# Kernel optimization log

Hardware: AMD Instinct MI355X
Metric: run time of the kernel (lower is better)

The kernel has to match this reference:

```python
import jax, jax.numpy as jnp
import numpy as np

B, N, M, K = 4, 2048, 8192, 3          # batches, coarse pts/batch, fine pts/batch, knn k
C_IN, C_SKIP, H, C_OUT = 256, 128, 256, 128


def setup_inputs() -> dict:
    key = jax.random.key(0)
    ks = jax.random.split(key, 8)
    x = jax.random.normal(ks[0], (B * N, C_IN), jnp.float32)
    pos = jax.random.normal(ks[1], (B * N, 3), jnp.float32)
    batch = jnp.repeat(jnp.arange(B, dtype=jnp.int64), N)        # sorted, equal-sized batches
    x_skip = jax.random.normal(ks[2], (B * M, C_SKIP), jnp.float32)
    pos_skip = jax.random.normal(ks[3], (B * M, 3), jnp.float32)
    batch_skip = jnp.repeat(jnp.arange(B, dtype=jnp.int64), M)
    # MLP params: Linear(384->256) + ReLU + Linear(256->128)
    W1 = jax.random.normal(ks[4], (C_IN + C_SKIP, H), jnp.float32) / np.sqrt(C_IN + C_SKIP)
    b1 = jnp.zeros((H,), jnp.float32)
    W2 = jax.random.normal(ks[5], (H, C_OUT), jnp.float32) / np.sqrt(H)
    b2 = jnp.zeros((C_OUT,), jnp.float32)
    return {"x": x, "pos": pos, "x_skip": x_skip, "pos_skip": pos_skip,
            "W1": W1, "b1": b1, "W2": W2, "b2": b2,
            "batch": batch, "batch_skip": batch_skip}


def _knn_interpolate(x, pos, pos_skip):
    # x: [B*N, C], pos: [B*N, 3], pos_skip: [B*M, 3]; batches are equal-sized & sorted,
    # so per-batch kNN == reshape to [B, n, ...] (matches batch/batch_skip vectors).
    xb = x.reshape(B, N, C_IN)
    pb = pos.reshape(B, N, 3)
    qb = pos_skip.reshape(B, M, 3)
    # squared pairwise distances via GEMM expansion: [B, M, N]
    d2 = (jnp.sum(qb * qb, -1)[:, :, None]
          + jnp.sum(pb * pb, -1)[:, None, :]
          - 2.0 * jnp.einsum('bmd,bnd->bmn', qb, pb))
    neg_d2, idx = jax.lax.top_k(-d2, K)           # k smallest distances
    d2k = jnp.maximum(-neg_d2, 0.0)               # [B, M, K]
    w = 1.0 / (d2k + 1e-16)                       # inverse-squared-distance weights
    feats = xb[jnp.arange(B)[:, None, None], idx] # gather: [B, M, K, C]
    interp = jnp.sum(w[..., None] * feats, axis=2) / jnp.sum(w, axis=2)[..., None]
    return interp.reshape(B * M, C_IN)


def reference(x, pos, x_skip, pos_skip, W1, b1, W2, b2, batch, batch_skip):
    xi = _knn_interpolate(x, pos, pos_skip)              # [B*M, C_IN]
    h = jnp.concatenate([xi, x_skip], axis=1)            # [B*M, C_IN+C_SKIP]
    h = jax.nn.relu(h @ W1 + b1)
    out = h @ W2 + b2                                    # [B*M, C_OUT]
    return (out, pos_skip, batch_skip)
```

## Files before the change

kernel.cpp:

```cpp
#include <hip/hip_runtime.h>
#include <math.h>
#include <stdint.h>

#define Bn    4
#define Nn    2048
#define Mn    8192
#define CIN   256
#define CSKIP 128
#define HID   256
#define COUT  128
#define KTOT  384

typedef short bf16x8 __attribute__((ext_vector_type(8)));
typedef float f32x16 __attribute__((ext_vector_type(16)));

__device__ __forceinline__ ushort f2bf(float f) {
    union { float f; unsigned u; } v; v.f = f;
    return (ushort)((v.u + 0x7fffu + ((v.u >> 16) & 1u)) >> 16);
}

__global__ __launch_bounds__(256) void pack_pos4(
    const float* __restrict__ pos, float4* __restrict__ pos4)
{
    const int i = blockIdx.x * 256 + threadIdx.x;
    const float* p = pos + (size_t)i * 3;
    const float p0 = p[0], p1 = p[1], p2 = p[2];
    const float pp = __fadd_rn(__fadd_rn(__fmul_rn(p0, p0), __fmul_rn(p1, p1)),
                               __fmul_rn(p2, p2));
    pos4[i] = make_float4(2.0f * p0, 2.0f * p1, 2.0f * p2, pp);
}

#define INSERT3(kA, kB, kC, k)            \
    do {                                  \
        const double _t = fmax(kA, k);    \
        kA = fmin(kA, k);                 \
        const double _u = fmax(kB, _t);   \
        kB = fmin(kB, _t);                \
        kC = fmin(kC, _u);                \
    } while (0)

__global__ __launch_bounds__(256) void fused_mid(
    const float* __restrict__ x,
    const float4* __restrict__ pos4,
    const float* __restrict__ xs,
    const float* __restrict__ pos_skip,
    const float* __restrict__ W1, const float* __restrict__ W2,
    ushort* __restrict__ Abig,
    ushort* __restrict__ W1T, ushort* __restrict__ W2T,
    float* __restrict__ tail_dst)
{
    __shared__ double sKey[16][3][17];
    __shared__ int    sIdx[16][3];
    __shared__ float  sRW[16][3];

    const int bid = blockIdx.x;
    const int tid = threadIdx.x;

    if (bid >= 2048) {
        const int cb = bid - 2048;
        if (cb < 4096) {
            const int q   = cb * 256 + tid;
            const int row = q >> 5;
            const int cq  = (q & 31) * 4;
            const float4 v = *(const float4*)(xs + (size_t)row * CSKIP + cq);
            ushort4 o; o.x = f2bf(v.x); o.y = f2bf(v.y); o.z = f2bf(v.z); o.w = f2bf(v.w);
            *(ushort4*)(Abig + (size_t)row * KTOT + CIN + cq) = o;
        } else if (cb < 4192) {
            const int q  = (cb - 4096) * 256 + tid;
            const int n  = q / 96;
            const int kq = (q % 96) * 4;
            ushort4 o;
            o.x = f2bf(W1[(size_t)(kq + 0) * HID + n]);
            o.y = f2bf(W1[(size_t)(kq + 1) * HID + n]);
            o.z = f2bf(W1[(size_t)(kq + 2) * HID + n]);
            o.w = f2bf(W1[(size_t)(kq + 3) * HID + n]);
            *(ushort4*)(W1T + (size_t)n * KTOT + kq) = o;
        } else if (cb < 4224) {
            const int q  = (cb - 4192) * 256 + tid;
            const int n  = q >> 6;
            const int kq = (q & 63) * 4;
            ushort4 o;
            o.x = f2bf(W2[(size_t)(kq + 0) * COUT + n]);
            o.y = f2bf(W2[(size_t)(kq + 1) * COUT + n]);
            o.z = f2bf(W2[(size_t)(kq + 2) * COUT + n]);
            o.w = f2bf(W2[(size_t)(kq + 3) * COUT + n]);
            *(ushort4*)(W2T + (size_t)n * HID + kq) = o;
        } else {
            const int i = (cb - 4224) * 256 + tid;
            const int nPos = Bn * Mn * 3;
            if (i < nPos) tail_dst[i] = pos_skip[i];
            else          tail_dst[i] = (float)((i - nPos) >> 13);
        }
        return;
    }

    const int qloc   = tid & 15;
    const int chunk  = tid >> 4;
    const int blockQ = bid * 16;
    const int b      = blockQ / Mn;

    const int q = blockQ + qloc;
    const float* qp = pos_skip + (size_t)q * 3;
    const float q0 = qp[0], q1 = qp[1], q2 = qp[2];
    const float qq = __fadd_rn(__fadd_rn(__fmul_rn(q0, q0), __fmul_rn(q1, q1)),
                               __fmul_rn(q2, q2));

    const int base = chunk * 128;
    const float4* __restrict__ cp = pos4 + (size_t)b * Nn + base;

    double kA = INFINITY, kB = INFINITY, kC = INFINITY;
#pragma unroll 4
    for (int j = 0; j < 128; ++j) {
        const float4 P = cp[j];
        const float dot2 = __fadd_rn(__fadd_rn(__fmul_rn(q0, P.x), __fmul_rn(q1, P.y)),
                                     __fmul_rn(q2, P.z));
        const float d = __fsub_rn(__fadd_rn(qq, P.w), dot2);
        const double k = __longlong_as_double(
            __double_as_longlong((double)d) | (long long)(base + j));
        INSERT3(kA, kB, kC, k);
    }
    sKey[chunk][0][qloc] = kA;
    sKey[chunk][1][qloc] = kB;
    sKey[chunk][2][qloc] = kC;
    __syncthreads();

    if (tid < 16) {
        double mA = INFINITY, mB = INFINITY, mC = INFINITY;
#pragma unroll
        for (int c = 0; c < 16; ++c)
#pragma unroll
            for (int s = 0; s < 3; ++s) {
                const double k = sKey[c][s][tid];
                INSERT3(mA, mB, mC, k);
            }
        const long long ba = __double_as_longlong(mA);
        const long long bb = __double_as_longlong(mB);
        const long long bc = __double_as_longlong(mC);
        const float dA = (float)__longlong_as_double(ba & ~0x7FFll);
        const float dB = (float)__longlong_as_double(bb & ~0x7FFll);
        const float dC = (float)__longlong_as_double(bc & ~0x7FFll);
        const float w0 = 1.0f / (fmaxf(dA, 0.0f) + 1e-16f);
        const float w1 = 1.0f / (fmaxf(dB, 0.0f) + 1e-16f);
        const float w2 = 1.0f / (fmaxf(dC, 0.0f) + 1e-16f);
        const float rden = 1.0f / (w0 + w1 + w2);
        sIdx[tid][0] = (int)(ba & 0x7FF);
        sIdx[tid][1] = (int)(bb & 0x7FF);
        sIdx[tid][2] = (int)(bc & 0x7FF);
        sRW[tid][0] = w0 * rden; sRW[tid][1] = w1 * rden; sRW[tid][2] = w2 * rden;
    }
    __syncthreads();

    const int wave = tid >> 6, lane = tid & 63;
    const size_t xbase = (size_t)b * Nn * CIN;
    for (int j = 0; j < 4; ++j) {
        const int lq = wave * 4 + j;
        const int gq = blockQ + lq;
        const int i0 = sIdx[lq][0], i1 = sIdx[lq][1], i2 = sIdx[lq][2];
        const float w0 = sRW[lq][0], w1 = sRW[lq][1], w2 = sRW[lq][2];
        const float4 f0 = ((const float4*)(x + xbase + (size_t)i0 * CIN))[lane];
        const float4 f1 = ((const float4*)(x + xbase + (size_t)i1 * CIN))[lane];
        const float4 f2 = ((const float4*)(x + xbase + (size_t)i2 * CIN))[lane];
        ushort4 ov;
        ov.x = f2bf(fmaf(w2, f2.x, fmaf(w1, f1.x, w0 * f0.x)));
        ov.y = f2bf(fmaf(w2, f2.y, fmaf(w1, f1.y, w0 * f0.y)));
        ov.z = f2bf(fmaf(w2, f2.z, fmaf(w1, f1.z, w0 * f0.z)));
        ov.w = f2bf(fmaf(w2, f2.w, fmaf(w1, f1.w, w0 * f0.w)));
        *(ushort4*)(Abig + (size_t)gq * KTOT + lane * 4) = ov;
    }
}

__global__ __launch_bounds__(256, 1) void mlp_fused(
    const ushort* __restrict__ Abig,
    const ushort* __restrict__ W1T,
    const float*  __restrict__ b1,
    const ushort* __restrict__ W2T,
    const float*  __restrict__ b2,
    float* __restrict__ out)
{
    __shared__ ushort Ast[128 * 32];
    __shared__ ushort Bst[128 * 32];
    __shared__ ushort Hs [128 * 128];

    const int tid  = threadIdx.x;
    const int wave = tid >> 6, lane = tid & 63;
    const int wr = wave >> 1, wc = wave & 1;
    const int l31 = lane & 31, kc0 = lane >> 5;
    const long rowbase = (long)blockIdx.x * 128;

    const int sr0 = tid >> 2;
    const int ss0 = tid & 3;
    const int ssw = (ss0 ^ (sr0 & 3));

    f32x16 acc2[2][2];
#pragma unroll
    for (int i = 0; i < 2; ++i)
#pragma unroll
        for (int j = 0; j < 2; ++j)
#pragma unroll
            for (int e = 0; e < 16; ++e) acc2[i][j][e] = 0.0f;

    for (int nh = 0; nh < 2; ++nh) {
        f32x16 acc1[2][2];
#pragma unroll
        for (int i = 0; i < 2; ++i)
#pragma unroll
            for (int j = 0; j < 2; ++j)
#pragma unroll
                for (int e = 0; e < 16; ++e) acc1[i][j][e] = 0.0f;

        const ushort* Ab = Abig + (size_t)rowbase * KTOT;
        const ushort* Wb = W1T + (size_t)(nh * 128) * KTOT;

        uint4 ra0, ra1, rb0, rb1;
        ra0 = *(const uint4*)(Ab + (size_t)sr0 * KTOT + ss0 * 8);
        ra1 = *(const uint4*)(Ab + (size_t)(sr0 + 64) * KTOT + ss0 * 8);
        rb0 = *(const uint4*)(Wb + (size_t)sr0 * KTOT + ss0 * 8);
        rb1 = *(const uint4*)(Wb + (size_t)(sr0 + 64) * KTOT + ss0 * 8);

        for (int t = 0; t < 12; ++t) {
            __syncthreads();
            *(uint4*)&Ast[sr0 * 32 + (ssw << 3)]        = ra0;
            *(uint4*)&Ast[(sr0 + 64) * 32 + (ssw << 3)] = ra1;
            *(uint4*)&Bst[sr0 * 32 + (ssw << 3)]        = rb0;
            *(uint4*)&Bst[(sr0 + 64) * 32 + (ssw << 3)] = rb1;
            __syncthreads();
            if (t < 11) {
                const int kt = (t + 1) * 32;
                ra0 = *(const uint4*)(Ab + (size_t)sr0 * KTOT + kt + ss0 * 8);
                ra1 = *(const uint4*)(Ab + (size_t)(sr0 + 64) * KTOT + kt + ss0 * 8);
                rb0 = *(const uint4*)(Wb + (size_t)sr0 * KTOT + kt + ss0 * 8);
                rb1 = *(const uint4*)(Wb + (size_t)(sr0 + 64) * KTOT + kt + ss0 * 8);
            }
#pragma unroll
            for (int s = 0; s < 2; ++s) {
                bf16x8 af[2], bq[2];
#pragma unroll
                for (int mf = 0; mf < 2; ++mf) {
                    const int r = wr * 64 + mf * 32 + l31;
                    af[mf] = *(const bf16x8*)&Ast[r * 32 + ((((s << 1) | kc0) ^ (r & 3)) << 3)];
                }
#pragma unroll
                for (int nf = 0; nf < 2; ++nf) {
                    const int rn = wc * 64 + nf * 32 + l31;
                    bq[nf] = *(const bf16x8*)&Bst[rn * 32 + ((((s << 1) | kc0) ^ (rn & 3)) << 3)];
                }
#pragma unroll
                for (int mf = 0; mf < 2; ++mf)
#pragma unroll
                    for (int nf = 0; nf < 2; ++nf)
                        acc1[mf][nf] = __builtin_amdgcn_mfma_f32_32x32x16_bf16(
                            af[mf], bq[nf], acc1[mf][nf], 0, 0, 0);
            }
        }

#pragma unroll
        for (int mf = 0; mf < 2; ++mf)
#pragma unroll
            for (int nf = 0; nf < 2; ++nf) {
                const int col = wc * 64 + nf * 32 + l31;
                const float b1v = b1[nh * 128 + col];
#pragma unroll
                for (int e = 0; e < 16; ++e) {
                    const int rl = wr * 64 + mf * 32 + (e & 3) + ((e >> 2) << 3) + (kc0 << 2);
                    const float hv = fmaxf(acc1[mf][nf][e] + b1v, 0.0f);
                    Hs[rl * 128 + (((col >> 3) ^ (rl & 7)) << 3) + (col & 7)] = f2bf(hv);
                }
            }
        __syncthreads();

        uint4 rw0, rw1;
        rw0 = *(const uint4*)(W2T + (size_t)sr0 * HID + nh * 128 + ss0 * 8);
        rw1 = *(const uint4*)(W2T + (size_t)(sr0 + 64) * HID + nh * 128 + ss0 * 8);

        for (int t = 0; t < 4; ++t) {
            __syncthreads();
            *(uint4*)&Bst[sr0 * 32 + (ssw << 3)]        = rw0;
            *(uint4*)&Bst[(sr0 + 64) * 32 + (ssw << 3)] = rw1;
            __syncthreads();
            if (t < 3) {
                const int kt = nh * 128 + (t + 1) * 32;
                rw0 = *(const uint4*)(W2T + (size_t)sr0 * HID + kt + ss0 * 8);
                rw1 = *(const uint4*)(W2T + (size_t)(sr0 + 64) * HID + kt + ss0 * 8);
            }
#pragma unroll
            for (int s = 0; s < 2; ++s) {
                bf16x8 af[2], bq[2];
#pragma unroll
                for (int mf = 0; mf < 2; ++mf) {
                    const int r  = wr * 64 + mf * 32 + l31;
                    const int kc = (t << 2) + (s << 1) + kc0;
                    af[mf] = *(const bf16x8*)&Hs[r * 128 + ((kc ^ (r & 7)) << 3)];
                }
#pragma unroll
                for (int nf = 0; nf < 2; ++nf) {
                    const int rn = wc * 64 + nf * 32 + l31;
                    bq[nf] = *(const bf16x8*)&Bst[rn * 32 + ((((s << 1) | kc0) ^ (rn & 3)) << 3)];
                }
#pragma unroll
                for (int mf = 0; mf < 2; ++mf)
#pragma unroll
                    for (int nf = 0; nf < 2; ++nf)
                        acc2[mf][nf] = __builtin_amdgcn_mfma_f32_32x32x16_bf16(
                            af[mf], bq[nf], acc2[mf][nf], 0, 0, 0);
            }
        }
        __syncthreads();
    }

#pragma unroll
    for (int mf = 0; mf < 2; ++mf)
#pragma unroll
        for (int nf = 0; nf < 2; ++nf) {
            const int col = wc * 64 + nf * 32 + l31;
            const float b2v = b2[col];
#pragma unroll
            for (int e = 0; e < 16; ++e) {
                const int rl = wr * 64 + mf * 32 + (e & 3) + ((e >> 2) << 3) + (kc0 << 2);
                out[(rowbase + rl) * COUT + col] = acc2[mf][nf][e] + b2v;
            }
        }
}

extern "C" void kernel_launch(void* const* d_in, const int* in_sizes, int n_in,
                              void* d_out, int out_size, void* d_ws, size_t ws_size,
                              hipStream_t stream)
{
    const float* x        = (const float*)d_in[0];
    const float* pos      = (const float*)d_in[1];
    const float* x_skip   = (const float*)d_in[2];
    const float* pos_skip = (const float*)d_in[3];
    const float* W1       = (const float*)d_in[4];
    const float* b1       = (const float*)d_in[5];
    const float* W2       = (const float*)d_in[6];
    const float* b2       = (const float*)d_in[7];

    float* out = (float*)d_out;

    ushort* Abig = (ushort*)d_ws;
    ushort* W1T  = (ushort*)((char*)d_ws + (size_t)Bn * Mn * KTOT * 2);
    ushort* W2T  = (ushort*)((char*)W1T + (size_t)HID * KTOT * 2);
    float4* pos4 = (float4*)((char*)W2T + (size_t)COUT * HID * 2);

    pack_pos4<<<dim3(Bn * Nn / 256), 256, 0, stream>>>(pos, pos4);

    fused_mid<<<dim3(2048 + 4736), 256, 0, stream>>>(
        x, pos4, x_skip, pos_skip, W1, W2, Abig, W1T, W2T,
        out + (size_t)Bn * Mn * COUT);

    mlp_fused<<<dim3(Bn * Mn / 128), 256, 0, stream>>>(
        Abig, W1T, b1, W2T, b2, out);
}
```

Baseline: 78.47 us.

## Apply W1 before interpolation: project coarse features, then interpolate hidden activations

Since interpolation is linear, the first linear layer is moved ahead of the kNN gather. x (8192 rows) and x_skip are multiplied by their slices of W1 in a separate GEMM kernel, and the kNN kernel then interpolates the projected Y rows, adds Z and b1, and applies ReLU. This cuts the first GEMM's work on the 32768 fine rows from K=384 to K=128. The price is that the fused MLP is split into four launches with bf16 intermediates Y, Z and h written to and read from global memory, and rounding differs because interpolation now happens on bf16-rounded projections.

```diff
diff --git a/kernel.cpp b/kernel.cpp
--- a/kernel.cpp
+++ b/kernel.cpp
@@ -18,16 +18,9 @@
     union { float f; unsigned u; } v; v.f = f;
     return (ushort)((v.u + 0x7fffu + ((v.u >> 16) & 1u)) >> 16);
 }
-
-__global__ __launch_bounds__(256) void pack_pos4(
-    const float* __restrict__ pos, float4* __restrict__ pos4)
-{
-    const int i = blockIdx.x * 256 + threadIdx.x;
-    const float* p = pos + (size_t)i * 3;
-    const float p0 = p[0], p1 = p[1], p2 = p[2];
-    const float pp = __fadd_rn(__fadd_rn(__fmul_rn(p0, p0), __fmul_rn(p1, p1)),
-                               __fmul_rn(p2, p2));
-    pos4[i] = make_float4(2.0f * p0, 2.0f * p1, 2.0f * p2, pp);
+__device__ __forceinline__ float bf2f(ushort u) {
+    union { unsigned u; float f; } v; v.u = ((unsigned)u) << 16;
+    return v.f;
 }
 
 #define INSERT3(kA, kB, kC, k)            \
@@ -39,64 +32,181 @@
         kC = fmin(kC, _u);                \
     } while (0)
 
-__global__ __launch_bounds__(256) void fused_mid(
-    const float* __restrict__ x,
+__global__ __launch_bounds__(256) void prep_kernel(
+    const float* __restrict__ x, const float* __restrict__ xs,
+    const float* __restrict__ pos, const float* __restrict__ pos_skip,
+    const float* __restrict__ W1, const float* __restrict__ W2,
+    ushort* __restrict__ xb, ushort* __restrict__ xsb,
+    ushort* __restrict__ W1T, ushort* __restrict__ W2T,
+    float4* __restrict__ pos4, float* __restrict__ tail_dst)
+{
+    const int bid = blockIdx.x, tid = threadIdx.x;
+    if (bid < 2048) {
+        const int q   = bid * 256 + tid;
+        const int row = q >> 6;
+        const int cq  = (q & 63) * 4;
+        const float4 v = *(const float4*)(x + (size_t)row * CIN + cq);
+        ushort4 o; o.x = f2bf(v.x); o.y = f2bf(v.y); o.z = f2bf(v.z); o.w = f2bf(v.w);
+        *(ushort4*)(xb + (size_t)row * CIN + cq) = o;
+    } else if (bid < 6144) {
+        const int q   = (bid - 2048) * 256 + tid;
+        const int row = q >> 5;
+        const int cq  = (q & 31) * 4;
+        const float4 v = *(const float4*)(xs + (size_t)row * CSKIP + cq);
+        ushort4 o; o.x = f2bf(v.x); o.y = f2bf(v.y); o.z = f2bf(v.z); o.w = f2bf(v.w);
+        *(ushort4*)(xsb + (size_t)row * CSKIP + cq) = o;
+    } else if (bid < 6240) {
+        const int q  = (bid - 6144) * 256 + tid;
+        const int n  = q / 96;
+        const int kq = (q % 96) * 4;
+        ushort4 o;
+        o.x = f2bf(W1[(size_t)(kq + 0) * HID + n]);
+        o.y = f2bf(W1[(size_t)(kq + 1) * HID + n]);
+        o.z = f2bf(W1[(size_t)(kq + 2) * HID + n]);
+        o.w = f2bf(W1[(size_t)(kq + 3) * HID + n]);
+        *(ushort4*)(W1T + (size_t)n * KTOT + kq) = o;
+    } else if (bid < 6272) {
+        const int q  = (bid - 6240) * 256 + tid;
+        const int n  = q >> 6;
+        const int kq = (q & 63) * 4;
+        ushort4 o;
+        o.x = f2bf(W2[(size_t)(kq + 0) * COUT + n]);
+        o.y = f2bf(W2[(size_t)(kq + 1) * COUT + n]);
+        o.z = f2bf(W2[(size_t)(kq + 2) * COUT + n]);
+        o.w = f2bf(W2[(size_t)(kq + 3) * COUT + n]);
+        *(ushort4*)(W2T + (size_t)n * HID + kq) = o;
+    } else if (bid < 6304) {
+        const int i = (bid - 6272) * 256 + tid;
+        const float* p = pos + (size_t)i * 3;
+        const float p0 = p[0], p1 = p[1], p2 = p[2];
+        const float pp = __fadd_rn(__fadd_rn(__fmul_rn(p0, p0), __fmul_rn(p1, p1)),
+                                   __fmul_rn(p2, p2));
+        pos4[i] = make_float4(2.0f * p0, 2.0f * p1, 2.0f * p2, pp);
+    } else {
+        const int i = (bid - 6304) * 256 + tid;
+        const int nPos = Bn * Mn * 3;
+        if (i < nPos) tail_dst[i] = pos_skip[i];
+        else          tail_dst[i] = (float)((i - nPos) >> 13);
+    }
+}
+
+__device__ __forceinline__ void gemm_acc128(
+    const ushort* __restrict__ A, int lda,
+    const ushort* __restrict__ BT, int ldb,
+    int ksteps, long rowbase, long colbase, int tid,
+    ushort* Ast, ushort* Bst, f32x16 acc[2][2])
+{
+    const int wave = tid >> 6, lane = tid & 63;
+    const int wr = wave >> 1, wc = wave & 1;
+    const int l31 = lane & 31, kc0 = lane >> 5;
+    const int sr0 = tid >> 2;
+    const int ss0 = tid & 3;
+    const int ssw = ss0 ^ (sr0 & 3);
+
+    uint4 ra0, ra1, rb0, rb1;
+    ra0 = *(const uint4*)(A + (rowbase + sr0) * lda + ss0 * 8);
+    ra1 = *(const uint4*)(A + (rowbase + sr0 + 64) * lda + ss0 * 8);
+    rb0 = *(const uint4*)(BT + (colbase + sr0) * ldb + ss0 * 8);
+    rb1 = *(const uint4*)(BT + (colbase + sr0 + 64) * ldb + ss0 * 8);
+
+    for (int t = 0; t < ksteps; ++t) {
+        __syncthreads();
+        *(uint4*)&Ast[sr0 * 32 + (ssw << 3)]        = ra0;
+        *(uint4*)&Ast[(sr0 + 64) * 32 + (ssw << 3)] = ra1;
+        *(uint4*)&Bst[sr0 * 32 + (ssw << 3)]        = rb0;
+        *(uint4*)&Bst[(sr0 + 64) * 32 + (ssw << 3)] = rb1;
+        __syncthreads();
+        if (t < ksteps - 1) {
+            const int kt = (t + 1) * 32;
+            ra0 = *(const uint4*)(A + (rowbase + sr0) * lda + kt + ss0 * 8);
+            ra1 = *(const uint4*)(A + (rowbase + sr0 + 64) * lda + kt + ss0 * 8);
+            rb0 = *(const uint4*)(BT + (colbase + sr0) * ldb + kt + ss0 * 8);
+            rb1 = *(const uint4*)(BT + (colbase + sr0 + 64) * ldb + kt + ss0 * 8);
+        }
+#pragma unroll
+        for (int s = 0; s < 2; ++s) {
+            bf16x8 af[2], bq[2];
+#pragma unroll
+            for (int mf = 0; mf < 2; ++mf) {
+                const int r = wr * 64 + mf * 32 + l31;
+                af[mf] = *(const bf16x8*)&Ast[r * 32 + ((((s << 1) | kc0) ^ (r & 3)) << 3)];
+            }
+#pragma unroll
+            for (int nf = 0; nf < 2; ++nf) {
+                const int rn = wc * 64 + nf * 32 + l31;
+                bq[nf] = *(const bf16x8*)&Bst[rn * 32 + ((((s << 1) | kc0) ^ (rn & 3)) << 3)];
+            }
+#pragma unroll
+            for (int mf = 0; mf < 2; ++mf)
+#pragma unroll
+                for (int nf = 0; nf < 2; ++nf)
+                    acc[mf][nf] = __builtin_amdgcn_mfma_f32_32x32x16_bf16(
+                        af[mf], bq[nf], acc[mf][nf], 0, 0, 0);
+        }
+    }
+}
+
+__global__ __launch_bounds__(256) void yz_gemm(
+    const ushort* __restrict__ xb, const ushort* __restrict__ xsb,
+    const ushort* __restrict__ W1T,
+    ushort* __restrict__ Y, ushort* __restrict__ Z)
+{
+    __shared__ ushort Ast[128 * 32];
+    __shared__ ushort Bst[128 * 32];
+
+    const int bid = blockIdx.x, tid = threadIdx.x;
+    f32x16 acc[2][2];
+#pragma unroll
+    for (int i = 0; i < 2; ++i)
+#pragma unroll
+        for (int j = 0; j < 2; ++j)
+#pragma unroll
+            for (int e = 0; e < 16; ++e) acc[i][j][e] = 0.0f;
+
+    const ushort* A; ushort* C;
+    long rowbase, colbase; int lda, ksteps; const ushort* BT; int ldb = KTOT;
+    if (bid < 128) {
+        rowbase = (long)(bid >> 1) * 128; colbase = (long)(bid & 1) * 128;
+        A = xb; lda = CIN; ksteps = CIN / 32; BT = W1T; C = Y;
+    } else {
+        const int cb = bid - 128;
+        rowbase = (long)(cb >> 1) * 128; colbase = (long)(cb & 1) * 128;
+        A = xsb; lda = CSKIP; ksteps = CSKIP / 32; BT = W1T + CIN; C = Z;
+    }
+    gemm_acc128(A, lda, BT, ldb, ksteps, rowbase, colbase, tid, Ast, Bst, acc);
+
+    const int wave = tid >> 6, lane = tid & 63;
+    const int wr = wave >> 1, wc = wave & 1;
+    const int l31 = lane & 31, kc0 = lane >> 5;
+#pragma unroll
+    for (int mf = 0; mf < 2; ++mf)
+#pragma unroll
+        for (int nf = 0; nf < 2; ++nf) {
+            const long col = colbase + wc * 64 + nf * 32 + l31;
+#pragma unroll
+            for (int e = 0; e < 16; ++e) {
+                const int rl = wr * 64 + mf * 32 + (e & 3) + ((e >> 2) << 3) + (kc0 << 2);
+                C[(rowbase + rl) * HID + col] = f2bf(acc[mf][nf][e]);
+            }
+        }
+}
+
+__global__ __launch_bounds__(256) void knn_h(
     const float4* __restrict__ pos4,
-    const float* __restrict__ xs,
     const float* __restrict__ pos_skip,
-    const float* __restrict__ W1, const float* __restrict__ W2,
-    ushort* __restrict__ Abig,
-    ushort* __restrict__ W1T, ushort* __restrict__ W2T,
-    float* __restrict__ tail_dst)
+    const ushort* __restrict__ Y,
+    const ushort* __restrict__ Z,
+    const float* __restrict__ b1,
+    ushort* __restrict__ h)
 {
     __shared__ double sKey[16][3][17];
     __shared__ int    sIdx[16][3];
     __shared__ float  sRW[16][3];
 
-    const int bid = blockIdx.x;
-    const int tid = threadIdx.x;
-
-    if (bid >= 2048) {
-        const int cb = bid - 2048;
-        if (cb < 4096) {
-            const int q   = cb * 256 + tid;
-            const int row = q >> 5;
-            const int cq  = (q & 31) * 4;
-            const float4 v = *(const float4*)(xs + (size_t)row * CSKIP + cq);
-            ushort4 o; o.x = f2bf(v.x); o.y = f2bf(v.y); o.z = f2bf(v.z); o.w = f2bf(v.w);
-            *(ushort4*)(Abig + (size_t)row * KTOT + CIN + cq) = o;
-        } else if (cb < 4192) {
-            const int q  = (cb - 4096) * 256 + tid;
-            const int n  = q / 96;
-            const int kq = (q % 96) * 4;
-            ushort4 o;
-            o.x = f2bf(W1[(size_t)(kq + 0) * HID + n]);
-            o.y = f2bf(W1[(size_t)(kq + 1) * HID + n]);
-            o.z = f2bf(W1[(size_t)(kq + 2) * HID + n]);
-            o.w = f2bf(W1[(size_t)(kq + 3) * HID + n]);
-            *(ushort4*)(W1T + (size_t)n * KTOT + kq) = o;
-        } else if (cb < 4224) {
-            const int q  = (cb - 4192) * 256 + tid;
-            const int n  = q >> 6;
-            const int kq = (q & 63) * 4;
-            ushort4 o;
-            o.x = f2bf(W2[(size_t)(kq + 0) * COUT + n]);
-            o.y = f2bf(W2[(size_t)(kq + 1) * COUT + n]);
-            o.z = f2bf(W2[(size_t)(kq + 2) * COUT + n]);
-            o.w = f2bf(W2[(size_t)(kq + 3) * COUT + n]);
-            *(ushort4*)(W2T + (size_t)n * HID + kq) = o;
-        } else {
-            const int i = (cb - 4224) * 256 + tid;
-            const int nPos = Bn * Mn * 3;
-            if (i < nPos) tail_dst[i] = pos_skip[i];
-            else          tail_dst[i] = (float)((i - nPos) >> 13);
-        }
-        return;
-    }
-
+    const int tid    = threadIdx.x;
     const int qloc   = tid & 15;
     const int chunk  = tid >> 4;
-    const int blockQ = bid * 16;
+    const int blockQ = blockIdx.x * 16;
     const int b      = blockQ / Mn;
 
     const int q = blockQ + qloc;
@@ -108,7 +218,7 @@
     const int base = chunk * 128;
     const float4* __restrict__ cp = pos4 + (size_t)b * Nn + base;
 
-    double kA = INFINITY, kB = INFINITY, kC = INFINITY;
+    double kA = (double)INFINITY, kB = (double)INFINITY, kC = (double)INFINITY;
 #pragma unroll 4
     for (int j = 0; j < 128; ++j) {
         const float4 P = cp[j];
@@ -125,7 +235,7 @@
     __syncthreads();
 
     if (tid < 16) {
-        double mA = INFINITY, mB = INFINITY, mC = INFINITY;
+        double mA = (double)INFINITY, mB = (double)INFINITY, mC = (double)INFINITY;
 #pragma unroll
         for (int c = 0; c < 16; ++c)
 #pragma unroll
@@ -151,162 +261,55 @@
     __syncthreads();
 
     const int wave = tid >> 6, lane = tid & 63;
-    const size_t xbase = (size_t)b * Nn * CIN;
+    const size_t ybase = (size_t)b * Nn;
+    const float4 b1v = ((const float4*)b1)[lane];
     for (int j = 0; j < 4; ++j) {
         const int lq = wave * 4 + j;
         const int gq = blockQ + lq;
         const int i0 = sIdx[lq][0], i1 = sIdx[lq][1], i2 = sIdx[lq][2];
         const float w0 = sRW[lq][0], w1 = sRW[lq][1], w2 = sRW[lq][2];
-        const float4 f0 = ((const float4*)(x + xbase + (size_t)i0 * CIN))[lane];
-        const float4 f1 = ((const float4*)(x + xbase + (size_t)i1 * CIN))[lane];
-        const float4 f2 = ((const float4*)(x + xbase + (size_t)i2 * CIN))[lane];
+        const ushort4 y0 = ((const ushort4*)(Y + (ybase + i0) * HID))[lane];
+        const ushort4 y1 = ((const ushort4*)(Y + (ybase + i1) * HID))[lane];
+        const ushort4 y2 = ((const ushort4*)(Y + (ybase + i2) * HID))[lane];
+        const ushort4 zz = ((const ushort4*)(Z + (size_t)gq * HID))[lane];
         ushort4 ov;
-        ov.x = f2bf(fmaf(w2, f2.x, fmaf(w1, f1.x, w0 * f0.x)));
-        ov.y = f2bf(fmaf(w2, f2.y, fmaf(w1, f1.y, w0 * f0.y)));
-        ov.z = f2bf(fmaf(w2, f2.z, fmaf(w1, f1.z, w0 * f0.z)));
-        ov.w = f2bf(fmaf(w2, f2.w, fmaf(w1, f1.w, w0 * f0.w)));
-        *(ushort4*)(Abig + (size_t)gq * KTOT + lane * 4) = ov;
-    }
-}
-
-__global__ __launch_bounds__(256, 1) void mlp_fused(
-    const ushort* __restrict__ Abig,
-    const ushort* __restrict__ W1T,
-    const float*  __restrict__ b1,
-    const ushort* __restrict__ W2T,
-    const float*  __restrict__ b2,
-    float* __restrict__ out)
+        {
+            float v;
+            v = fmaf(w2, bf2f(y2.x), fmaf(w1, bf2f(y1.x), w0 * bf2f(y0.x))) + bf2f(zz.x) + b1v.x;
+            ov.x = f2bf(fmaxf(v, 0.0f));
+            v = fmaf(w2, bf2f(y2.y), fmaf(w1, bf2f(y1.y), w0 * bf2f(y0.y))) + bf2f(zz.y) + b1v.y;
+            ov.y = f2bf(fmaxf(v, 0.0f));
+            v = fmaf(w2, bf2f(y2.z), fmaf(w1, bf2f(y1.z), w0 * bf2f(y0.z))) + bf2f(zz.z) + b1v.z;
+            ov.z = f2bf(fmaxf(v, 0.0f));
+            v = fmaf(w2, bf2f(y2.w), fmaf(w1, bf2f(y1.w), w0 * bf2f(y0.w))) + bf2f(zz.w) + b1v.w;
+            ov.w = f2bf(fmaxf(v, 0.0f));
+        }
+        *(ushort4*)(h + (size_t)gq * HID + lane * 4) = ov;
+    }
+}
+
+__global__ __launch_bounds__(256) void gemm2(
+    const ushort* __restrict__ h, const ushort* __restrict__ W2T,
+    const float* __restrict__ b2, float* __restrict__ out)
 {
     __shared__ ushort Ast[128 * 32];
     __shared__ ushort Bst[128 * 32];
-    __shared__ ushort Hs [128 * 128];
-
-    const int tid  = threadIdx.x;
+
+    const int tid = threadIdx.x;
+    f32x16 acc[2][2];
+#pragma unroll
+    for (int i = 0; i < 2; ++i)
+#pragma unroll
+        for (int j = 0; j < 2; ++j)
+#pragma unroll
+            for (int e = 0; e < 16; ++e) acc[i][j][e] = 0.0f;
+
+    const long rowbase = (long)blockIdx.x * 128;
+    gemm_acc128(h, HID, W2T, HID, HID / 32, rowbase, 0, tid, Ast, Bst, acc);
+
     const int wave = tid >> 6, lane = tid & 63;
     const int wr = wave >> 1, wc = wave & 1;
     const int l31 = lane & 31, kc0 = lane >> 5;
-    const long rowbase = (long)blockIdx.x * 128;
-
-    const int sr0 = tid >> 2;
-    const int ss0 = tid & 3;
-    const int ssw = (ss0 ^ (sr0 & 3));
-
-    f32x16 acc2[2][2];
-#pragma unroll
-    for (int i = 0; i < 2; ++i)
-#pragma unroll
-        for (int j = 0; j < 2; ++j)
-#pragma unroll
-            for (int e = 0; e < 16; ++e) acc2[i][j][e] = 0.0f;
-
-    for (int nh = 0; nh < 2; ++nh) {
-        f32x16 acc1[2][2];
-#pragma unroll
-        for (int i = 0; i < 2; ++i)
-#pragma unroll
-            for (int j = 0; j < 2; ++j)
-#pragma unroll
-                for (int e = 0; e < 16; ++e) acc1[i][j][e] = 0.0f;
-
-        const ushort* Ab = Abig + (size_t)rowbase * KTOT;
-        const ushort* Wb = W1T + (size_t)(nh * 128) * KTOT;
-
-        uint4 ra0, ra1, rb0, rb1;
-        ra0 = *(const uint4*)(Ab + (size_t)sr0 * KTOT + ss0 * 8);
-        ra1 = *(const uint4*)(Ab + (size_t)(sr0 + 64) * KTOT + ss0 * 8);
-        rb0 = *(const uint4*)(Wb + (size_t)sr0 * KTOT + ss0 * 8);
-        rb1 = *(const uint4*)(Wb + (size_t)(sr0 + 64) * KTOT + ss0 * 8);
-
-        for (int t = 0; t < 12; ++t) {
-            __syncthreads();
-            *(uint4*)&Ast[sr0 * 32 + (ssw << 3)]        = ra0;
-            *(uint4*)&Ast[(sr0 + 64) * 32 + (ssw << 3)] = ra1;
-            *(uint4*)&Bst[sr0 * 32 + (ssw << 3)]        = rb0;
-            *(uint4*)&Bst[(sr0 + 64) * 32 + (ssw << 3)] = rb1;
-            __syncthreads();
-            if (t < 11) {
-                const int kt = (t + 1) * 32;
-                ra0 = *(const uint4*)(Ab + (size_t)sr0 * KTOT + kt + ss0 * 8);
-                ra1 = *(const uint4*)(Ab + (size_t)(sr0 + 64) * KTOT + kt + ss0 * 8);
-                rb0 = *(const uint4*)(Wb + (size_t)sr0 * KTOT + kt + ss0 * 8);
-                rb1 = *(const uint4*)(Wb + (size_t)(sr0 + 64) * KTOT + kt + ss0 * 8);
-            }
-#pragma unroll
-            for (int s = 0; s < 2; ++s) {
-                bf16x8 af[2], bq[2];
-#pragma unroll
-                for (int mf = 0; mf < 2; ++mf) {
-                    const int r = wr * 64 + mf * 32 + l31;
-                    af[mf] = *(const bf16x8*)&Ast[r * 32 + ((((s << 1) | kc0) ^ (r & 3)) << 3)];
-                }
-#pragma unroll
-                for (int nf = 0; nf < 2; ++nf) {
-                    const int rn = wc * 64 + nf * 32 + l31;
-                    bq[nf] = *(const bf16x8*)&Bst[rn * 32 + ((((s << 1) | kc0) ^ (rn & 3)) << 3)];
-                }
-#pragma unroll
-                for (int mf = 0; mf < 2; ++mf)
-#pragma unroll
-                    for (int nf = 0; nf < 2; ++nf)
-                        acc1[mf][nf] = __builtin_amdgcn_mfma_f32_32x32x16_bf16(
-                            af[mf], bq[nf], acc1[mf][nf], 0, 0, 0);
-            }
-        }
-
-#pragma unroll
-        for (int mf = 0; mf < 2; ++mf)
-#pragma unroll
-            for (int nf = 0; nf < 2; ++nf) {
-                const int col = wc * 64 + nf * 32 + l31;
-                const float b1v = b1[nh * 128 + col];
-#pragma unroll
-                for (int e = 0; e < 16; ++e) {
-                    const int rl = wr * 64 + mf * 32 + (e & 3) + ((e >> 2) << 3) + (kc0 << 2);
-                    const float hv = fmaxf(acc1[mf][nf][e] + b1v, 0.0f);
-                    Hs[rl * 128 + (((col >> 3) ^ (rl & 7)) << 3) + (col & 7)] = f2bf(hv);
-                }
-            }
-        __syncthreads();
-
-        uint4 rw0, rw1;
-        rw0 = *(const uint4*)(W2T + (size_t)sr0 * HID + nh * 128 + ss0 * 8);
-        rw1 = *(const uint4*)(W2T + (size_t)(sr0 + 64) * HID + nh * 128 + ss0 * 8);
-
-        for (int t = 0; t < 4; ++t) {
-            __syncthreads();
-            *(uint4*)&Bst[sr0 * 32 + (ssw << 3)]        = rw0;
-            *(uint4*)&Bst[(sr0 + 64) * 32 + (ssw << 3)] = rw1;
-            __syncthreads();
-            if (t < 3) {
-                const int kt = nh * 128 + (t + 1) * 32;
-                rw0 = *(const uint4*)(W2T + (size_t)sr0 * HID + kt + ss0 * 8);
-                rw1 = *(const uint4*)(W2T + (size_t)(sr0 + 64) * HID + kt + ss0 * 8);
-            }
-#pragma unroll
-            for (int s = 0; s < 2; ++s) {
-                bf16x8 af[2], bq[2];
-#pragma unroll
-                for (int mf = 0; mf < 2; ++mf) {
-                    const int r  = wr * 64 + mf * 32 + l31;
-                    const int kc = (t << 2) + (s << 1) + kc0;
-                    af[mf] = *(const bf16x8*)&Hs[r * 128 + ((kc ^ (r & 7)) << 3)];
-                }
-#pragma unroll
-                for (int nf = 0; nf < 2; ++nf) {
-                    const int rn = wc * 64 + nf * 32 + l31;
-                    bq[nf] = *(const bf16x8*)&Bst[rn * 32 + ((((s << 1) | kc0) ^ (rn & 3)) << 3)];
-                }
-#pragma unroll
-                for (int mf = 0; mf < 2; ++mf)
-#pragma unroll
-                    for (int nf = 0; nf < 2; ++nf)
-                        acc2[mf][nf] = __builtin_amdgcn_mfma_f32_32x32x16_bf16(
-                            af[mf], bq[nf], acc2[mf][nf], 0, 0, 0);
-            }
-        }
-        __syncthreads();
-    }
-
 #pragma unroll
     for (int mf = 0; mf < 2; ++mf)
 #pragma unroll
@@ -316,7 +319,7 @@
 #pragma unroll
             for (int e = 0; e < 16; ++e) {
                 const int rl = wr * 64 + mf * 32 + (e & 3) + ((e >> 2) << 3) + (kc0 << 2);
-                out[(rowbase + rl) * COUT + col] = acc2[mf][nf][e] + b2v;
+                out[(rowbase + rl) * COUT + col] = acc[mf][nf][e] + b2v;
             }
         }
 }
@@ -336,17 +339,23 @@
 
     float* out = (float*)d_out;
 
-    ushort* Abig = (ushort*)d_ws;
-    ushort* W1T  = (ushort*)((char*)d_ws + (size_t)Bn * Mn * KTOT * 2);
-    ushort* W2T  = (ushort*)((char*)W1T + (size_t)HID * KTOT * 2);
-    float4* pos4 = (float4*)((char*)W2T + (size_t)COUT * HID * 2);
-
-    pack_pos4<<<dim3(Bn * Nn / 256), 256, 0, stream>>>(pos, pos4);
-
-    fused_mid<<<dim3(2048 + 4736), 256, 0, stream>>>(
-        x, pos4, x_skip, pos_skip, W1, W2, Abig, W1T, W2T,
+    char* wp = (char*)d_ws;
+    ushort* xb  = (ushort*)wp; wp += (size_t)Bn * Nn * CIN * 2;
+    ushort* xsb = (ushort*)wp; wp += (size_t)Bn * Mn * CSKIP * 2;
+    ushort* Yb  = (ushort*)wp; wp += (size_t)Bn * Nn * HID * 2;
+    ushort* Zb  = (ushort*)wp; wp += (size_t)Bn * Mn * HID * 2;
+    ushort* hb  = (ushort*)wp; wp += (size_t)Bn * Mn * HID * 2;
+    ushort* W1T = (ushort*)wp; wp += (size_t)HID * KTOT * 2;
+    ushort* W2T = (ushort*)wp; wp += (size_t)COUT * HID * 2;
+    float4* pos4 = (float4*)wp;
+
+    prep_kernel<<<dim3(6816), 256, 0, stream>>>(
+        x, x_skip, pos, pos_skip, W1, W2, xb, xsb, W1T, W2T, pos4,
         out + (size_t)Bn * Mn * COUT);
 
-    mlp_fused<<<dim3(Bn * Mn / 128), 256, 0, stream>>>(
-        Abig, W1T, b1, W2T, b2, out);
-}
+    yz_gemm<<<dim3(640), 256, 0, stream>>>(xb, xsb, W1T, Yb, Zb);
+
+    knn_h<<<dim3(2048), 256, 0, stream>>>(pos4, pos_skip, Yb, Zb, b1, hb);
+
+    gemm2<<<dim3(256), 256, 0, stream>>>(hb, W2T, b2, out);
+}
```

After: 77.79 us. No clear change (-0.9%).
